# Performance work log

Hardware: AMD Instinct MI355X
Metric: run time of the kernel (lower is better)

The kernel has to match this reference:

```python
import jax, jax.numpy as jnp
import numpy as np

DIM = 768
HEADS = 12
HEAD_DIM = DIM // HEADS
B, N = 4, 2048


def setup_inputs() -> dict:
    key = jax.random.key(0)
    ks = jax.random.split(key, 5)
    s = 0.02
    return {
        "x": jax.random.normal(ks[0], (B, N, DIM), dtype=jnp.float32),
        "w_qkv": jax.random.normal(ks[1], (DIM, 3 * DIM), dtype=jnp.float32) * s,
        "b_qkv": jnp.zeros((3 * DIM,), dtype=jnp.float32),
        "w_proj": jax.random.normal(ks[2], (DIM, DIM), dtype=jnp.float32) * s,
        "b_proj": jnp.zeros((DIM,), dtype=jnp.float32),
    }


def reference(x, w_qkv, b_qkv, w_proj, b_proj):
    b, n, c = x.shape
    scale = HEAD_DIM ** -0.5
    qkv = x @ w_qkv + b_qkv                       # [B,N,3C]
    qkv = qkv.reshape(b, n, 3, HEADS, HEAD_DIM)
    q = qkv[:, :, 0].transpose(0, 2, 1, 3)        # [B,H,N,D]
    k = qkv[:, :, 1].transpose(0, 2, 1, 3)
    v = qkv[:, :, 2].transpose(0, 2, 1, 3)
    attn = jnp.einsum("bhqd,bhkd->bhqk", q, k) * scale
    attn = jax.nn.softmax(attn, axis=-1)
    out = jnp.einsum("bhqk,bhkd->bhqd", attn, v)  # [B,H,N,D]
    out = out.transpose(0, 2, 1, 3).reshape(b, n, c)
    return out @ w_proj + b_proj
```

## Files before the change

kernel.cpp:

```cpp
#include <hip/hip_runtime.h>

typedef short sh8 __attribute__((ext_vector_type(8)));
typedef short sh4 __attribute__((ext_vector_type(4)));
typedef float f32x4 __attribute__((ext_vector_type(4)));
typedef float f32x16 __attribute__((ext_vector_type(16)));
typedef unsigned u32x4 __attribute__((ext_vector_type(4)));

extern "C" __device__ float __ocml_native_exp2_f32(float);

__device__ __forceinline__ short f2bf(float f) {
  unsigned u = __builtin_bit_cast(unsigned, f);
  u += 0x7fffu + ((u >> 16) & 1u);
  return (short)(u >> 16);
}

__device__ __forceinline__ void gload16(const short* g, short* l) {
  __builtin_amdgcn_global_load_lds(
      (const __attribute__((address_space(1))) unsigned*)g,
      (__attribute__((address_space(3))) unsigned*)l, 16, 0, 0);
}

__device__ __forceinline__ void wait4_barrier() {
  asm volatile("s_waitcnt vmcnt(4)" ::: "memory");
  __builtin_amdgcn_s_barrier();
  asm volatile("" ::: "memory");
}
__device__ __forceinline__ void wait0_barrier() {
  asm volatile("s_waitcnt vmcnt(0)" ::: "memory");
  __builtin_amdgcn_s_barrier();
  asm volatile("" ::: "memory");
}

__device__ __forceinline__ int xcd_swizzle(int bidl, int nwg) {
  int q = nwg >> 3, rr = nwg & 7;
  int xcd = bidl & 7, idx = bidl >> 3;
  return (xcd < rr ? xcd * (q + 1) : rr * (q + 1) + (xcd - rr) * q) + idx;
}

__global__ void cast_f32_bf16(const float* __restrict__ in, short* __restrict__ out, int n) {
  int i = (blockIdx.x * blockDim.x + threadIdx.x) * 4;
  if (i >= n) return;
  float4 f = *(const float4*)(in + i);
  sh4 o;
  o.x = f2bf(f.x); o.y = f2bf(f.y); o.z = f2bf(f.z); o.w = f2bf(f.w);
  *(sh4*)(out + i) = o;
}

__global__ __launch_bounds__(256) void transpose_cast_t(
    const float* __restrict__ in, short* __restrict__ out, int K, int Nn) {
  __shared__ short Tl[64][72];
  const int t = threadIdx.x;
  const int n0 = blockIdx.x * 64, k0 = blockIdx.y * 64;
  const int kr0 = t >> 4;
  const int nc = (t & 15) * 4;
#pragma unroll
  for (int p = 0; p < 4; p++) {
    int kr = kr0 + p * 16;
    float4 f = *(const float4*)(in + (size_t)(k0 + kr) * Nn + n0 + nc);
    Tl[nc + 0][kr] = f2bf(f.x);
    Tl[nc + 1][kr] = f2bf(f.y);
    Tl[nc + 2][kr] = f2bf(f.z);
    Tl[nc + 3][kr] = f2bf(f.w);
  }
  __syncthreads();
  const int nr0 = t >> 3;
  const int kk = (t & 7) * 8;
#pragma unroll
  for (int p = 0; p < 2; p++) {
    int nr = nr0 + p * 32;
    *(sh8*)(out + (size_t)(n0 + nr) * K + k0 + kk) = *(const sh8*)&Tl[nr][kk];
  }
}

template <int OUTF32>
__global__ __launch_bounds__(256) void gemm_bt(
    const short* __restrict__ A, const short* __restrict__ Bt,
    const float* __restrict__ bias, void* __restrict__ Cv,
    int M, int Nn, int K) {
  __shared__ short As[3][128][32];
  __shared__ short Bs[3][128][32];
  const int t = threadIdx.x;
  const int wave = t >> 6, lane = t & 63, quad = lane >> 4, l15 = lane & 15;
  const int wm = (wave >> 1) * 64, wn = (wave & 1) * 64;
  const int nwg = gridDim.x * gridDim.y;
  const int wg = xcd_swizzle(blockIdx.y * gridDim.x + blockIdx.x, nwg);
  const int row0 = (wg / gridDim.x) * 128, col0 = (wg % gridDim.x) * 128;
  f32x4 acc[4][4] = {};

  const int srow = t >> 2;
  const int ssl = ((t & 3) ^ ((t >> 3) & 3)) * 8;
  const short* Asrc0 = A + (size_t)(row0 + srow) * K + ssl;
  const short* Asrc1 = A + (size_t)(row0 + 64 + srow) * K + ssl;
  const short* Bsrc0 = Bt + (size_t)(col0 + srow) * K + ssl;
  const short* Bsrc1 = Bt + (size_t)(col0 + 64 + srow) * K + ssl;
  short* AsF = &As[0][0][0];
  short* BsF = &Bs[0][0][0];
  const int wdst = wave * 512;

  const int soA = (quad ^ ((l15 >> 1) & 3)) * 8;

  const int T = K >> 5;
#pragma unroll
  for (int pt = 0; pt < 2; pt++) {
    short* Ad = AsF + pt * 4096 + wdst;
    short* Bd = BsF + pt * 4096 + wdst;
    const int k0 = pt * 32;
    gload16(Asrc0 + k0, Ad);
    gload16(Asrc1 + k0, Ad + 2048);
    gload16(Bsrc0 + k0, Bd);
    gload16(Bsrc1 + k0, Bd + 2048);
  }

  int rb = 0, wb = 2;
  for (int tt = 0; tt < T; tt++) {
    if (tt + 1 < T) wait4_barrier(); else wait0_barrier();
    if (tt + 2 < T) {
      const int k0 = (tt + 2) * 32;
      short* Ad = AsF + wb * 4096 + wdst;
      short* Bd = BsF + wb * 4096 + wdst;
      gload16(Asrc0 + k0, Ad);
      gload16(Asrc1 + k0, Ad + 2048);
      gload16(Bsrc0 + k0, Bd);
      gload16(Bsrc1 + k0, Bd + 2048);
    }
    const short* Ab = AsF + rb * 4096;
    const short* Bb = BsF + rb * 4096;
    sh8 af[4], bfv[4];
#pragma unroll
    for (int i = 0; i < 4; i++) af[i] = *(const sh8*)&Ab[(wm + i * 16 + l15) * 32 + soA];
#pragma unroll
    for (int j = 0; j < 4; j++) bfv[j] = *(const sh8*)&Bb[(wn + j * 16 + l15) * 32 + soA];
#pragma unroll
    for (int i = 0; i < 4; i++)
#pragma unroll
      for (int j = 0; j < 4; j++)
        acc[i][j] = __builtin_amdgcn_mfma_f32_16x16x32_bf16(af[i], bfv[j], acc[i][j], 0, 0, 0);
    rb = rb == 2 ? 0 : rb + 1;
    wb = wb == 2 ? 0 : wb + 1;
  }

#pragma unroll
  for (int i = 0; i < 4; i++)
#pragma unroll
    for (int j = 0; j < 4; j++) {
      int r = row0 + wm + i * 16 + quad * 4;
      int c = col0 + wn + j * 16 + l15;
      float bv = bias[c];
#pragma unroll
      for (int e = 0; e < 4; e++) {
        float v = acc[i][j][e] + bv;
        if (OUTF32)
          ((float*)Cv)[(size_t)(r + e) * Nn + c] = v;
        else
          ((short*)Cv)[(size_t)(r + e) * Nn + c] = f2bf(v);
      }
    }
}

__global__ __launch_bounds__(256) void gemm_qkv(
    const short* __restrict__ A, const short* __restrict__ Bt,
    const float* __restrict__ bias,
    short* __restrict__ Qh, short* __restrict__ Kh, short* __restrict__ VhT) {
  const int K = 768;
  __shared__ short SMEM[24576];
  const int t = threadIdx.x;
  const int wave = t >> 6, lane = t & 63, quad = lane >> 4, l15 = lane & 15;
  const int wm = (wave >> 1) * 64, wn = (wave & 1) * 64;
  const int nwg = gridDim.x * gridDim.y;
  const int wg = xcd_swizzle(blockIdx.y * gridDim.x + blockIdx.x, nwg);
  const int row0 = (wg / gridDim.x) * 128, col0 = (wg % gridDim.x) * 128;
  f32x4 acc[4][4] = {};

  const int srow = t >> 2;
  const int ssl = ((t & 3) ^ ((t >> 3) & 3)) * 8;
  const short* Asrc0 = A + (size_t)(row0 + srow) * K + ssl;
  const short* Asrc1 = A + (size_t)(row0 + 64 + srow) * K + ssl;
  const short* Bsrc0 = Bt + (size_t)(col0 + srow) * K + ssl;
  const short* Bsrc1 = Bt + (size_t)(col0 + 64 + srow) * K + ssl;
  short* AsF = SMEM;
  short* BsF = SMEM + 12288;
  const int wdst = wave * 512;

  const int soA = (quad ^ ((l15 >> 1) & 3)) * 8;

  const int T = K >> 5;
#pragma unroll
  for (int pt = 0; pt < 2; pt++) {
    short* Ad = AsF + pt * 4096 + wdst;
    short* Bd = BsF + pt * 4096 + wdst;
    const int k0 = pt * 32;
    gload16(Asrc0 + k0, Ad);
    gload16(Asrc1 + k0, Ad + 2048);
    gload16(Bsrc0 + k0, Bd);
    gload16(Bsrc1 + k0, Bd + 2048);
  }

  int rb = 0, wb = 2;
  for (int tt = 0; tt < T; tt++) {
    if (tt + 1 < T) wait4_barrier(); else wait0_barrier();
    if (tt + 2 < T) {
      const int k0 = (tt + 2) * 32;
      short* Ad = AsF + wb * 4096 + wdst;
      short* Bd = BsF + wb * 4096 + wdst;
      gload16(Asrc0 + k0, Ad);
      gload16(Asrc1 + k0, Ad + 2048);
      gload16(Bsrc0 + k0, Bd);
      gload16(Bsrc1 + k0, Bd + 2048);
    }
    const short* Ab = AsF + rb * 4096;
    const short* Bb = BsF + rb * 4096;
    sh8 af[4], bfv[4];
#pragma unroll
    for (int i = 0; i < 4; i++) af[i] = *(const sh8*)&Ab[(wm + i * 16 + l15) * 32 + soA];
#pragma unroll
    for (int j = 0; j < 4; j++) bfv[j] = *(const sh8*)&Bb[(wn + j * 16 + l15) * 32 + soA];
#pragma unroll
    for (int i = 0; i < 4; i++)
#pragma unroll
      for (int j = 0; j < 4; j++)
        acc[i][j] = __builtin_amdgcn_mfma_f32_16x16x32_bf16(af[i], bfv[j], acc[i][j], 0, 0, 0);
    rb = rb == 2 ? 0 : rb + 1;
    wb = wb == 2 ? 0 : wb + 1;
  }

  const int s = col0 >= 1536 ? 2 : (col0 >= 768 ? 1 : 0);

  if (s < 2) {
    short* dst = s == 0 ? Qh : Kh;
    const float scl = (s == 0) ? 0.18033688011112042f : 1.0f;
#pragma unroll
    for (int j = 0; j < 4; j++) {
      int c = col0 + wn + j * 16 + l15;
      int hd = c - s * 768;
      int h = hd >> 6;
      float bv = bias[c];
#pragma unroll
      for (int i = 0; i < 4; i++) {
        int rbase = row0 + wm + i * 16 + quad * 4;
#pragma unroll
        for (int e = 0; e < 4; e++) {
          int r = rbase + e;
          int b = r >> 11, n = r & 2047;
          float v = (acc[i][j][e] + bv) * scl;
          dst[(size_t)(b * 12 + h) * 131072 + n * 64 + (hd & 63)] = f2bf(v);
        }
      }
    }
  } else {
    __syncthreads();
    short* Tl = SMEM;
#pragma unroll
    for (int j = 0; j < 4; j++) {
      int cl = wn + j * 16 + l15;
      float bv = bias[col0 + cl];
#pragma unroll
      for (int i = 0; i < 4; i++) {
        int rl = wm + i * 16 + quad * 4;
        sh4 pk;
#pragma unroll
        for (int e = 0; e < 4; e++) pk[e] = f2bf(acc[i][j][e] + bv);
        *(sh4*)&Tl[cl * 136 + rl] = pk;
      }
    }
    __syncthreads();
    const int b = row0 >> 11, n0 = row0 & 2047;
    const int h0 = (col0 - 1536) >> 6;
#pragma unroll
    for (int p = 0; p < 8; p++) {
      int cl = (t >> 4) + p * 16;
      int nn = (t & 15) * 8;
      int hg = h0 + (cl >> 6);
      int d = cl & 63;
      sh8 vv = *(const sh8*)&Tl[cl * 136 + nn];
      *(sh8*)&VhT[(size_t)(b * 12 + hg) * 131072 + (size_t)d * 2048 + n0 + nn] = vv;
    }
  }
}

__global__ __launch_bounds__(256, 3) void attn7(const short* __restrict__ Qh,
                                                const short* __restrict__ Kh,
                                                const short* __restrict__ VhT,
                                                short* __restrict__ outb) {
  const int bid = blockIdx.x;
  const int qb = bid / 48;
  const int bh = bid - qb * 48;
  const int t = threadIdx.x;
  const int w = t >> 6, lane = t & 63;
  const int l31 = lane & 31, hi = lane >> 5;

  __shared__ short Kl[3][64][64];
  __shared__ short Vt[3][64][64];

  const size_t hb = (size_t)bh * 131072;

  sh8 qa[4];
  {
    const short* qp = Qh + hb + (size_t)(qb * 128 + w * 32 + l31) * 64 + hi * 8;
    qa[0] = *(const sh8*)(qp);
    qa[1] = *(const sh8*)(qp + 16);
    qa[2] = *(const sh8*)(qp + 32);
    qa[3] = *(const sh8*)(qp + 48);
  }
  asm volatile("s_waitcnt vmcnt(0)" ::: "memory");

  f32x16 o[2] = {};
  f32x4 lsv = {};

  const int srow = t >> 3;
  const int ssl = ((t & 7) ^ (srow & 7)) * 8;
  const short* Ksrc = Kh + hb + (size_t)srow * 64 + ssl;
  const short* Vsrc = VhT + hb + (size_t)srow * 2048 + ssl;
  short* KlF = &Kl[0][0][0];
  short* VtF = &Vt[0][0][0];
  const int wdst = w * 512;

  const int sw7 = l31 & 7;
  int rsl[4];
#pragma unroll
  for (int ks = 0; ks < 4; ks++) rsl[ks] = (((ks << 1) | hi) ^ sw7) * 8;

#pragma unroll
  for (int pt = 0; pt < 2; pt++) {
    const int key0 = pt * 64;
    short* Kd = KlF + pt * 4096 + wdst;
    short* Vd = VtF + pt * 4096 + wdst;
    gload16(Ksrc + (size_t)key0 * 64, Kd);
    gload16(Ksrc + (size_t)(key0 + 32) * 64, Kd + 2048);
    gload16(Vsrc + key0, Vd);
    gload16(Vsrc + (size_t)32 * 2048 + key0, Vd + 2048);
  }

  int rb = 0, wb = 2;
  for (int kt = 0; kt < 32; kt++) {
    if (kt < 31) wait4_barrier(); else wait0_barrier();
    if (kt < 30) {
      const int key0 = (kt + 2) * 64;
      short* Kd = KlF + wb * 4096 + wdst;
      short* Vd = VtF + wb * 4096 + wdst;
      gload16(Ksrc + (size_t)key0 * 64, Kd);
      gload16(Ksrc + (size_t)(key0 + 32) * 64, Kd + 2048);
      gload16(Vsrc + key0, Vd);
      gload16(Vsrc + (size_t)32 * 2048 + key0, Vd + 2048);
    }

    const short* Kb = KlF + rb * 4096;
    const short* Vb = VtF + rb * 4096;

    sh8 pa[4];
#pragma unroll
    for (int kb = 0; kb < 2; kb++) {
      const short* kr = Kb + (kb * 32 + l31) * 64;
      f32x16 s = {};
#pragma unroll
      for (int ks = 0; ks < 4; ks++)
        s = __builtin_amdgcn_mfma_f32_32x32x16_bf16(*(const sh8*)(kr + rsl[ks]), qa[ks], s, 0, 0, 0);
      unsigned u[8];
#pragma unroll
      for (int m = 0; m < 8; m++) {
        float e0 = __ocml_native_exp2_f32(s[2 * m]);
        float e1 = __ocml_native_exp2_f32(s[2 * m + 1]);
        lsv[m & 3] += e0 + e1;
        asm("v_cvt_pk_bf16_f32 %0, %1, %2" : "=v"(u[m]) : "v"(e0), "v"(e1));
      }
      unsigned y0 = (unsigned)__shfl_xor((int)(hi ? u[0] : u[2]), 32, 64);
      unsigned y1 = (unsigned)__shfl_xor((int)(hi ? u[1] : u[3]), 32, 64);
      unsigned y2 = (unsigned)__shfl_xor((int)(hi ? u[4] : u[6]), 32, 64);
      unsigned y3 = (unsigned)__shfl_xor((int)(hi ? u[5] : u[7]), 32, 64);
      unsigned w0 = hi ? y0 : u[0];
      unsigned w1 = hi ? y1 : u[1];
      unsigned w2 = hi ? u[2] : y0;
      unsigned w3 = hi ? u[3] : y1;
      unsigned w4 = hi ? y2 : u[4];
      unsigned w5 = hi ? y3 : u[5];
      unsigned w6 = hi ? u[6] : y2;
      unsigned w7 = hi ? u[7] : y3;
      u32x4 A0 = {w0, w1, w2, w3};
      u32x4 A1 = {w4, w5, w6, w7};
      pa[2 * kb] = __builtin_bit_cast(sh8, A0);
      pa[2 * kb + 1] = __builtin_bit_cast(sh8, A1);
    }

    __builtin_amdgcn_s_setprio(1);
#pragma unroll
    for (int db = 0; db < 2; db++) {
      const short* vr = Vb + (db * 32 + l31) * 64;
#pragma unroll
      for (int ks = 0; ks < 4; ks++)
        o[db] = __builtin_amdgcn_mfma_f32_32x32x16_bf16(pa[ks], *(const sh8*)(vr + rsl[ks]), o[db], 0, 0, 0);
    }
    __builtin_amdgcn_s_setprio(0);
    rb = rb == 2 ? 0 : rb + 1;
    wb = wb == 2 ? 0 : wb + 1;
  }

  float ls = lsv[0] + lsv[1] + lsv[2] + lsv[3];
  ls += __shfl_xor(ls, 32, 64);
  float inv = 1.f / ls;

  const int b = bh / 12, hh = bh - b * 12;
#pragma unroll
  for (int r = 0; r < 16; r++) {
    int qr = (r & 3) + 8 * (r >> 2) + 4 * hi;
    float iv = __shfl(inv, qr, 64);
    int n = qb * 128 + w * 32 + qr;
    short* op = outb + (size_t)(b * 2048 + n) * 768 + hh * 64 + l31;
    op[0] = f2bf(o[0][r] * iv);
    op[32] = f2bf(o[1][r] * iv);
  }
}

extern "C" void kernel_launch(void* const* d_in, const int* in_sizes, int n_in,
                              void* d_out, int out_size, void* d_ws, size_t ws_size,
                              hipStream_t stream) {
  const float* x = (const float*)d_in[0];
  const float* w_qkv = (const float*)d_in[1];
  const float* b_qkv = (const float*)d_in[2];
  const float* w_proj = (const float*)d_in[3];
  const float* b_proj = (const float*)d_in[4];
  float* out = (float*)d_out;

  char* p = (char*)d_ws;
  short* xb = (short*)p;     p += (size_t)8192 * 768 * 2;
  short* wqkvT = (short*)p;  p += (size_t)2304 * 768 * 2;
  short* wprojT = (short*)p; p += (size_t)768 * 768 * 2;
  short* Qh = (short*)p;     p += (size_t)48 * 131072 * 2;
  short* Kh = (short*)p;     p += (size_t)48 * 131072 * 2;
  short* VhT = (short*)p;    p += (size_t)48 * 131072 * 2;
  short* attnb = (short*)p;  p += (size_t)8192 * 768 * 2;

  cast_f32_bf16<<<(8192 * 768 / 4) / 256, 256, 0, stream>>>(x, xb, 8192 * 768);
  {
    dim3 gt(2304 / 64, 768 / 64);
    transpose_cast_t<<<gt, 256, 0, stream>>>(w_qkv, wqkvT, 768, 2304);
  }
  {
    dim3 gt(768 / 64, 768 / 64);
    transpose_cast_t<<<gt, 256, 0, stream>>>(w_proj, wprojT, 768, 768);
  }

  dim3 g1(2304 / 128, 8192 / 128);
  gemm_qkv<<<g1, 256, 0, stream>>>(xb, wqkvT, b_qkv, Qh, Kh, VhT);

  attn7<<<16 * 48, 256, 0, stream>>>(Qh, Kh, VhT, attnb);

  dim3 g2(768 / 128, 8192 / 128);
  gemm_bt<1><<<g2, 256, 0, stream>>>(attnb, wprojT, b_proj, out, 8192, 768, 768);
}
```

Before: 223.8 us.

## Shrink LDS staging to triple-buffer A/K and double-buffer B/V for occupancy

In both GEMMs and the attention kernel, the second operand (B tile or V tile) now uses two LDS buffers instead of three and is prefetched one step ahead, while A/K keeps three buffers and a two-step prefetch. This cuts shared memory per block from 48KB to 40KB, so launch bounds can ask for 4 blocks per CU instead of 3 in attention. The cost is a shorter prefetch distance for B/V, with a vmcnt(2) wait, which may expose more load latency. It may also tighten register budgets.

```diff
diff --git a/kernel.cpp b/kernel.cpp
--- a/kernel.cpp
+++ b/kernel.cpp
@@ -20,8 +20,8 @@
       (__attribute__((address_space(3))) unsigned*)l, 16, 0, 0);
 }
 
-__device__ __forceinline__ void wait4_barrier() {
-  asm volatile("s_waitcnt vmcnt(4)" ::: "memory");
+__device__ __forceinline__ void wait2_barrier() {
+  asm volatile("s_waitcnt vmcnt(2)" ::: "memory");
   __builtin_amdgcn_s_barrier();
   asm volatile("" ::: "memory");
 }
@@ -73,96 +73,11 @@
 }
 
 template <int OUTF32>
-__global__ __launch_bounds__(256) void gemm_bt(
+__global__ __launch_bounds__(256, 4) void gemm_bt(
     const short* __restrict__ A, const short* __restrict__ Bt,
     const float* __restrict__ bias, void* __restrict__ Cv,
     int M, int Nn, int K) {
-  __shared__ short As[3][128][32];
-  __shared__ short Bs[3][128][32];
-  const int t = threadIdx.x;
-  const int wave = t >> 6, lane = t & 63, quad = lane >> 4, l15 = lane & 15;
-  const int wm = (wave >> 1) * 64, wn = (wave & 1) * 64;
-  const int nwg = gridDim.x * gridDim.y;
-  const int wg = xcd_swizzle(blockIdx.y * gridDim.x + blockIdx.x, nwg);
-  const int row0 = (wg / gridDim.x) * 128, col0 = (wg % gridDim.x) * 128;
-  f32x4 acc[4][4] = {};
-
-  const int srow = t >> 2;
-  const int ssl = ((t & 3) ^ ((t >> 3) & 3)) * 8;
-  const short* Asrc0 = A + (size_t)(row0 + srow) * K + ssl;
-  const short* Asrc1 = A + (size_t)(row0 + 64 + srow) * K + ssl;
-  const short* Bsrc0 = Bt + (size_t)(col0 + srow) * K + ssl;
-  const short* Bsrc1 = Bt + (size_t)(col0 + 64 + srow) * K + ssl;
-  short* AsF = &As[0][0][0];
-  short* BsF = &Bs[0][0][0];
-  const int wdst = wave * 512;
-
-  const int soA = (quad ^ ((l15 >> 1) & 3)) * 8;
-
-  const int T = K >> 5;
-#pragma unroll
-  for (int pt = 0; pt < 2; pt++) {
-    short* Ad = AsF + pt * 4096 + wdst;
-    short* Bd = BsF + pt * 4096 + wdst;
-    const int k0 = pt * 32;
-    gload16(Asrc0 + k0, Ad);
-    gload16(Asrc1 + k0, Ad + 2048);
-    gload16(Bsrc0 + k0, Bd);
-    gload16(Bsrc1 + k0, Bd + 2048);
-  }
-
-  int rb = 0, wb = 2;
-  for (int tt = 0; tt < T; tt++) {
-    if (tt + 1 < T) wait4_barrier(); else wait0_barrier();
-    if (tt + 2 < T) {
-      const int k0 = (tt + 2) * 32;
-      short* Ad = AsF + wb * 4096 + wdst;
-      short* Bd = BsF + wb * 4096 + wdst;
-      gload16(Asrc0 + k0, Ad);
-      gload16(Asrc1 + k0, Ad + 2048);
-      gload16(Bsrc0 + k0, Bd);
-      gload16(Bsrc1 + k0, Bd + 2048);
-    }
-    const short* Ab = AsF + rb * 4096;
-    const short* Bb = BsF + rb * 4096;
-    sh8 af[4], bfv[4];
-#pragma unroll
-    for (int i = 0; i < 4; i++) af[i] = *(const sh8*)&Ab[(wm + i * 16 + l15) * 32 + soA];
-#pragma unroll
-    for (int j = 0; j < 4; j++) bfv[j] = *(const sh8*)&Bb[(wn + j * 16 + l15) * 32 + soA];
-#pragma unroll
-    for (int i = 0; i < 4; i++)
-#pragma unroll
-      for (int j = 0; j < 4; j++)
-        acc[i][j] = __builtin_amdgcn_mfma_f32_16x16x32_bf16(af[i], bfv[j], acc[i][j], 0, 0, 0);
-    rb = rb == 2 ? 0 : rb + 1;
-    wb = wb == 2 ? 0 : wb + 1;
-  }
-
-#pragma unroll
-  for (int i = 0; i < 4; i++)
-#pragma unroll
-    for (int j = 0; j < 4; j++) {
-      int r = row0 + wm + i * 16 + quad * 4;
-      int c = col0 + wn + j * 16 + l15;
-      float bv = bias[c];
-#pragma unroll
-      for (int e = 0; e < 4; e++) {
-        float v = acc[i][j][e] + bv;
-        if (OUTF32)
-          ((float*)Cv)[(size_t)(r + e) * Nn + c] = v;
-        else
-          ((short*)Cv)[(size_t)(r + e) * Nn + c] = f2bf(v);
-      }
-    }
-}
-
-__global__ __launch_bounds__(256) void gemm_qkv(
-    const short* __restrict__ A, const short* __restrict__ Bt,
-    const float* __restrict__ bias,
-    short* __restrict__ Qh, short* __restrict__ Kh, short* __restrict__ VhT) {
-  const int K = 768;
-  __shared__ short SMEM[24576];
+  __shared__ short SMEM[20480];
   const int t = threadIdx.x;
   const int wave = t >> 6, lane = t & 63, quad = lane >> 4, l15 = lane & 15;
   const int wm = (wave >> 1) * 64, wn = (wave & 1) * 64;
@@ -184,31 +99,113 @@
   const int soA = (quad ^ ((l15 >> 1) & 3)) * 8;
 
   const int T = K >> 5;
-#pragma unroll
-  for (int pt = 0; pt < 2; pt++) {
-    short* Ad = AsF + pt * 4096 + wdst;
-    short* Bd = BsF + pt * 4096 + wdst;
-    const int k0 = pt * 32;
-    gload16(Asrc0 + k0, Ad);
-    gload16(Asrc1 + k0, Ad + 2048);
-    gload16(Bsrc0 + k0, Bd);
-    gload16(Bsrc1 + k0, Bd + 2048);
-  }
-
-  int rb = 0, wb = 2;
+  gload16(Asrc0, AsF + wdst);
+  gload16(Asrc1, AsF + 2048 + wdst);
+  gload16(Bsrc0, BsF + wdst);
+  gload16(Bsrc1, BsF + 2048 + wdst);
+  gload16(Asrc0 + 32, AsF + 4096 + wdst);
+  gload16(Asrc1 + 32, AsF + 4096 + 2048 + wdst);
+
+  int ra = 0, wa = 2;
   for (int tt = 0; tt < T; tt++) {
-    if (tt + 1 < T) wait4_barrier(); else wait0_barrier();
+    if (tt + 1 < T) wait2_barrier(); else wait0_barrier();
+    if (tt + 1 < T) {
+      const int k0 = (tt + 1) * 32;
+      short* Bd = BsF + ((tt + 1) & 1) * 4096 + wdst;
+      gload16(Bsrc0 + k0, Bd);
+      gload16(Bsrc1 + k0, Bd + 2048);
+    }
     if (tt + 2 < T) {
       const int k0 = (tt + 2) * 32;
-      short* Ad = AsF + wb * 4096 + wdst;
-      short* Bd = BsF + wb * 4096 + wdst;
+      short* Ad = AsF + wa * 4096 + wdst;
       gload16(Asrc0 + k0, Ad);
       gload16(Asrc1 + k0, Ad + 2048);
+    }
+    const short* Ab = AsF + ra * 4096;
+    const short* Bb = BsF + (tt & 1) * 4096;
+    sh8 af[4], bfv[4];
+#pragma unroll
+    for (int i = 0; i < 4; i++) af[i] = *(const sh8*)&Ab[(wm + i * 16 + l15) * 32 + soA];
+#pragma unroll
+    for (int j = 0; j < 4; j++) bfv[j] = *(const sh8*)&Bb[(wn + j * 16 + l15) * 32 + soA];
+#pragma unroll
+    for (int i = 0; i < 4; i++)
+#pragma unroll
+      for (int j = 0; j < 4; j++)
+        acc[i][j] = __builtin_amdgcn_mfma_f32_16x16x32_bf16(af[i], bfv[j], acc[i][j], 0, 0, 0);
+    ra = ra == 2 ? 0 : ra + 1;
+    wa = wa == 2 ? 0 : wa + 1;
+  }
+
+#pragma unroll
+  for (int i = 0; i < 4; i++)
+#pragma unroll
+    for (int j = 0; j < 4; j++) {
+      int r = row0 + wm + i * 16 + quad * 4;
+      int c = col0 + wn + j * 16 + l15;
+      float bv = bias[c];
+#pragma unroll
+      for (int e = 0; e < 4; e++) {
+        float v = acc[i][j][e] + bv;
+        if (OUTF32)
+          ((float*)Cv)[(size_t)(r + e) * Nn + c] = v;
+        else
+          ((short*)Cv)[(size_t)(r + e) * Nn + c] = f2bf(v);
+      }
+    }
+}
+
+__global__ __launch_bounds__(256, 4) void gemm_qkv(
+    const short* __restrict__ A, const short* __restrict__ Bt,
+    const float* __restrict__ bias,
+    short* __restrict__ Qh, short* __restrict__ Kh, short* __restrict__ VhT) {
+  const int K = 768;
+  __shared__ short SMEM[20480];
+  const int t = threadIdx.x;
+  const int wave = t >> 6, lane = t & 63, quad = lane >> 4, l15 = lane & 15;
+  const int wm = (wave >> 1) * 64, wn = (wave & 1) * 64;
+  const int nwg = gridDim.x * gridDim.y;
+  const int wg = xcd_swizzle(blockIdx.y * gridDim.x + blockIdx.x, nwg);
+  const int row0 = (wg / gridDim.x) * 128, col0 = (wg % gridDim.x) * 128;
+  f32x4 acc[4][4] = {};
+
+  const int srow = t >> 2;
+  const int ssl = ((t & 3) ^ ((t >> 3) & 3)) * 8;
+  const short* Asrc0 = A + (size_t)(row0 + srow) * K + ssl;
+  const short* Asrc1 = A + (size_t)(row0 + 64 + srow) * K + ssl;
+  const short* Bsrc0 = Bt + (size_t)(col0 + srow) * K + ssl;
+  const short* Bsrc1 = Bt + (size_t)(col0 + 64 + srow) * K + ssl;
+  short* AsF = SMEM;
+  short* BsF = SMEM + 12288;
+  const int wdst = wave * 512;
+
+  const int soA = (quad ^ ((l15 >> 1) & 3)) * 8;
+
+  const int T = K >> 5;
+  gload16(Asrc0, AsF + wdst);
+  gload16(Asrc1, AsF + 2048 + wdst);
+  gload16(Bsrc0, BsF + wdst);
+  gload16(Bsrc1, BsF + 2048 + wdst);
+  gload16(Asrc0 + 32, AsF + 4096 + wdst);
+  gload16(Asrc1 + 32, AsF + 4096 + 2048 + wdst);
+
+  int ra = 0, wa = 2;
+  for (int tt = 0; tt < T; tt++) {
+    if (tt + 1 < T) wait2_barrier(); else wait0_barrier();
+    if (tt + 1 < T) {
+      const int k0 = (tt + 1) * 32;
+      short* Bd = BsF + ((tt + 1) & 1) * 4096 + wdst;
       gload16(Bsrc0 + k0, Bd);
       gload16(Bsrc1 + k0, Bd + 2048);
     }
-    const short* Ab = AsF + rb * 4096;
-    const short* Bb = BsF + rb * 4096;
+    if (tt + 2 < T) {
+      const int k0 = (tt + 2) * 32;
+      short* Ad = AsF + wa * 4096 + wdst;
+      gload16(Asrc0 + k0, Ad);
+      gload16(Asrc1 + k0, Ad + 2048);
+    }
+    const short* Ab = AsF + ra * 4096;
+    const short* Bb = BsF + (tt & 1) * 4096;
     sh8 af[4], bfv[4];
 #pragma unroll
     for (int i = 0; i < 4; i++) af[i] = *(const sh8*)&Ab[(wm + i * 16 + l15) * 32 + soA];
@@ -219,8 +216,8 @@
 #pragma unroll
       for (int j = 0; j < 4; j++)
         acc[i][j] = __builtin_amdgcn_mfma_f32_16x16x32_bf16(af[i], bfv[j], acc[i][j], 0, 0, 0);
-    rb = rb == 2 ? 0 : rb + 1;
-    wb = wb == 2 ? 0 : wb + 1;
+    ra = ra == 2 ? 0 : ra + 1;
+    wa = wa == 2 ? 0 : wa + 1;
   }
 
   const int s = col0 >= 1536 ? 2 : (col0 >= 768 ? 1 : 0);
@@ -277,7 +274,7 @@
   }
 }
 
-__global__ __launch_bounds__(256, 3) void attn7(const short* __restrict__ Qh,
+__global__ __launch_bounds__(256, 4) void attn8(const short* __restrict__ Qh,
                                                 const short* __restrict__ Kh,
                                                 const short* __restrict__ VhT,
                                                 short* __restrict__ outb) {
@@ -288,8 +285,7 @@
   const int w = t >> 6, lane = t & 63;
   const int l31 = lane & 31, hi = lane >> 5;
 
-  __shared__ short Kl[3][64][64];
-  __shared__ short Vt[3][64][64];
+  __shared__ short SM[20480];
 
   const size_t hb = (size_t)bh * 131072;
 
@@ -310,8 +306,8 @@
   const int ssl = ((t & 7) ^ (srow & 7)) * 8;
   const short* Ksrc = Kh + hb + (size_t)srow * 64 + ssl;
   const short* Vsrc = VhT + hb + (size_t)srow * 2048 + ssl;
-  short* KlF = &Kl[0][0][0];
-  short* VtF = &Vt[0][0][0];
+  short* KlF = SM;
+  short* VtF = SM + 12288;
   const int wdst = w * 512;
 
   const int sw7 = l31 & 7;
@@ -319,32 +315,31 @@
 #pragma unroll
   for (int ks = 0; ks < 4; ks++) rsl[ks] = (((ks << 1) | hi) ^ sw7) * 8;
 
-#pragma unroll
-  for (int pt = 0; pt < 2; pt++) {
-    const int key0 = pt * 64;
-    short* Kd = KlF + pt * 4096 + wdst;
-    short* Vd = VtF + pt * 4096 + wdst;
-    gload16(Ksrc + (size_t)key0 * 64, Kd);
-    gload16(Ksrc + (size_t)(key0 + 32) * 64, Kd + 2048);
-    gload16(Vsrc + key0, Vd);
-    gload16(Vsrc + (size_t)32 * 2048 + key0, Vd + 2048);
-  }
-
-  int rb = 0, wb = 2;
+  gload16(Ksrc, KlF + wdst);
+  gload16(Ksrc + (size_t)32 * 64, KlF + 2048 + wdst);
+  gload16(Vsrc, VtF + wdst);
+  gload16(Vsrc + (size_t)32 * 2048, VtF + 2048 + wdst);
+  gload16(Ksrc + (size_t)64 * 64, KlF + 4096 + wdst);
+  gload16(Ksrc + (size_t)96 * 64, KlF + 4096 + 2048 + wdst);
+
+  int rk = 0, wk = 2;
   for (int kt = 0; kt < 32; kt++) {
-    if (kt < 31) wait4_barrier(); else wait0_barrier();
-    if (kt < 30) {
+    if (kt < 31) wait2_barrier(); else wait0_barrier();
+    if (kt + 1 < 32) {
+      const int key0 = (kt + 1) * 64;
+      short* Vd = VtF + ((kt + 1) & 1) * 4096 + wdst;
+      gload16(Vsrc + key0, Vd);
+      gload16(Vsrc + (size_t)32 * 2048 + key0, Vd + 2048);
+    }
+    if (kt + 2 < 32) {
       const int key0 = (kt + 2) * 64;
-      short* Kd = KlF + wb * 4096 + wdst;
-      short* Vd = VtF + wb * 4096 + wdst;
+      short* Kd = KlF + wk * 4096 + wdst;
       gload16(Ksrc + (size_t)key0 * 64, Kd);
       gload16(Ksrc + (size_t)(key0 + 32) * 64, Kd + 2048);
-      gload16(Vsrc + key0, Vd);
-      gload16(Vsrc + (size_t)32 * 2048 + key0, Vd + 2048);
-    }
-
-    const short* Kb = KlF + rb * 4096;
-    const short* Vb = VtF + rb * 4096;
+    }
+
+    const short* Kb = KlF + rk * 4096;
+    const short* Vb = VtF + (kt & 1) * 4096;
 
     sh8 pa[4];
 #pragma unroll
@@ -389,8 +384,8 @@
         o[db] = __builtin_amdgcn_mfma_f32_32x32x16_bf16(pa[ks], *(const sh8*)(vr + rsl[ks]), o[db], 0, 0, 0);
     }
     __builtin_amdgcn_s_setprio(0);
-    rb = rb == 2 ? 0 : rb + 1;
-    wb = wb == 2 ? 0 : wb + 1;
+    rk = rk == 2 ? 0 : rk + 1;
+    wk = wk == 2 ? 0 : wk + 1;
   }
 
   float ls = lsv[0] + lsv[1] + lsv[2] + lsv[3];
@@ -441,7 +436,7 @@
   dim3 g1(2304 / 128, 8192 / 128);
   gemm_qkv<<<g1, 256, 0, stream>>>(xb, wqkvT, b_qkv, Qh, Kh, VhT);
 
-  attn7<<<16 * 48, 256, 0, stream>>>(Qh, Kh, VhT, attnb);
+  attn8<<<16 * 48, 256, 0, stream>>>(Qh, Kh, VhT, attnb);
 
   dim3 g2(768 / 128, 8192 / 128);
   gemm_bt<1><<<g2, 256, 0, stream>>>(attnb, wprojT, b_proj, out, 8192, 768, 768);
```

Result: faster. 215.9 us (-3.5%).
